# Performance work log

Measured on AMD Instinct MI355X. Metric: run time of the kernel, lower is better.

The kernel has to match this reference:

```python
import jax, jax.numpy as jnp
import numpy as np

TOPK = 2

def setup_inputs() -> dict:
    key = jax.random.key(0)
    k1, k2, k3, k4 = jax.random.split(key, 4)
    T, H, F, E = 2048, 1024, 4096, 8
    x = jax.random.normal(k1, (T, H), dtype=jnp.float32)
    router_weight = jax.random.normal(k2, (H, E), dtype=jnp.float32) * (1.0 / np.sqrt(H))
    w1 = jax.random.normal(k3, (E, H, F), dtype=jnp.float32) * (1.0 / np.sqrt(H))
    w2 = jax.random.normal(k4, (E, F, H), dtype=jnp.float32) * (1.0 / np.sqrt(F))
    return {"x": x, "router_weight": router_weight, "w1": w1, "w2": w2}


def reference(x, router_weight, w1, w2):
    # x: [T, H] tokens; w1: [E, H, F]; w2: [E, F, H]
    T, H = x.shape
    E = w1.shape[0]
    K = TOPK
    M = T * K  # total dispatched token copies

    # --- TopKRouter (Megatron default: top-k over logits, softmax over selected) ---
    logits = x @ router_weight                      # [T, E]
    top_logits, top_idx = jax.lax.top_k(logits, K)  # [T, K]
    probs = jax.nn.softmax(top_logits, axis=-1)     # [T, K]

    # --- AG-scatter: group token copies by expert (flux grouped-GEMM layout) ---
    flat_expert = top_idx.reshape(-1)               # [M], token-major
    token_id = jnp.repeat(jnp.arange(T), K)         # [M]
    order = jnp.argsort(flat_expert)                # stable sort by expert id
    xg = x[token_id[order]]                         # [M, H] grouped inputs
    eg = flat_expert[order]                         # [M] expert of each slot

    # --- grouped GEMM1 + fused GELU, grouped GEMM2 (exact, via expert masking) ---
    # Rows not belonging to expert e are zeroed; gelu(0)=0 and 0@w2=0, so the
    # accumulated buffers are exactly the grouped-GEMM results.
    gelu_buf = jnp.zeros((M, w1.shape[2]), dtype=x.dtype)
    y = jnp.zeros((M, H), dtype=x.dtype)
    for e in range(E):
        mask = (eg == e)[:, None].astype(x.dtype)
        ge = jax.nn.gelu((xg * mask) @ w1[e], approximate=False)  # [M, F]
        gelu_buf = gelu_buf + ge
        y = y + ge @ w2[e]

    # --- gather + reduce: weighted combine of the K expert outputs per token ---
    pg = probs.reshape(-1)[order]                   # [M]
    mlp_output = jax.ops.segment_sum(y * pg[:, None], token_id[order], num_segments=T)
    return (mlp_output, gelu_buf)
```

## Files before the change

### kernel.cpp

```cpp
#include <hip/hip_runtime.h>
#include <hip/hip_bf16.h>
#include <stdint.h>

typedef unsigned short u16;
typedef unsigned int u32;
typedef __attribute__((ext_vector_type(8))) short short8;
typedef __attribute__((ext_vector_type(4))) float f32x4;

#define T_TOK 2048
#define H_DIM 1024
#define F_DIM 4096
#define E_NUM 8
#define M_SLOT 4096
#define MAXTILES 40
#define KSPLIT 2

__device__ __forceinline__ u16 f2bf(float f){
  union { float f; u32 u; } v; v.f = f;
  return (u16)((v.u + 0x7FFFu + ((v.u >> 16) & 1u)) >> 16);
}

__device__ __forceinline__ void gload_lds16(const void* g, void* l){
  __builtin_amdgcn_global_load_lds(
      (const __attribute__((address_space(1))) u32*)g,
      (__attribute__((address_space(3))) u32*)l, 16, 0, 0);
}

__global__ __launch_bounds__(256) void router_kernel(
    const float* __restrict__ x, const float* __restrict__ rw,
    int* __restrict__ tok_e, float* __restrict__ tok_p){
  __shared__ float wlds[E_NUM * H_DIM];
  int tid = threadIdx.x;
  for (int i = tid; i < H_DIM * E_NUM; i += 256){
    int h = i >> 3, e = i & 7;
    wlds[e * H_DIM + h] = rw[i];
  }
  __syncthreads();
  int wave = tid >> 6, lane = tid & 63;
  int t = blockIdx.x * 4 + wave;
  const float* xr = x + (size_t)t * H_DIM;
  float acc[E_NUM];
  #pragma unroll
  for (int e = 0; e < E_NUM; e++) acc[e] = 0.f;
  for (int i = 0; i < H_DIM / 64; i++){
    float xv = xr[lane + 64 * i];
    #pragma unroll
    for (int e = 0; e < E_NUM; e++) acc[e] += xv * wlds[e * H_DIM + lane + 64 * i];
  }
  #pragma unroll
  for (int e = 0; e < E_NUM; e++){
    float r = acc[e];
    #pragma unroll
    for (int off = 32; off; off >>= 1) r += __shfl_xor(r, off, 64);
    acc[e] = r;
  }
  if (lane == 0){
    float l0 = acc[0]; int e0 = 0;
    #pragma unroll
    for (int e = 1; e < E_NUM; e++) if (acc[e] > l0){ l0 = acc[e]; e0 = e; }
    float l1 = -INFINITY; int e1 = 0;
    #pragma unroll
    for (int e = 0; e < E_NUM; e++) if (e != e0 && acc[e] > l1){ l1 = acc[e]; e1 = e; }
    float ex = expf(l1 - l0);
    float inv = 1.f / (1.f + ex);
    tok_e[2*t] = e0; tok_e[2*t+1] = e1;
    tok_p[2*t] = inv; tok_p[2*t+1] = ex * inv;
  }
}

__global__ void hist_kernel(const int* __restrict__ tok_e, u32* __restrict__ partial){
  int lane = threadIdx.x & 63;
  int m = blockIdx.x * 64 + lane;
  int e = tok_e[m];
  #pragma unroll
  for (int ee = 0; ee < E_NUM; ee++){
    unsigned long long mk = __ballot(e == ee);
    if (lane == ee) partial[blockIdx.x * E_NUM + ee] = (u32)__popcll(mk);
  }
}

__global__ void scan_kernel(const u32* __restrict__ partial, u32* __restrict__ baseb,
                            int4* __restrict__ tiles, int* __restrict__ ntiles){
  int lane = threadIdx.x;
  u32 exc[E_NUM], tot[E_NUM];
  #pragma unroll
  for (int e = 0; e < E_NUM; e++){
    u32 v = partial[lane * E_NUM + e];
    u32 own = v;
    #pragma unroll
    for (int off = 1; off < 64; off <<= 1){
      u32 tu = __shfl_up(v, off, 64);
      if (lane >= off) v += tu;
    }
    exc[e] = v - own;
    tot[e] = __shfl(v, 63, 64);
  }
  u32 offs[E_NUM + 1]; offs[0] = 0;
  #pragma unroll
  for (int e = 0; e < E_NUM; e++) offs[e+1] = offs[e] + tot[e];
  #pragma unroll
  for (int e = 0; e < E_NUM; e++) baseb[lane * E_NUM + e] = offs[e] + exc[e];
  if (lane == 0){
    int nt = 0;
    for (int e = 0; e < E_NUM; e++){
      int cnt = (int)tot[e];
      for (int r0 = 0; r0 < cnt; r0 += 128){
        tiles[nt] = make_int4((int)offs[e] + r0, min(128, cnt - r0), e, 0);
        nt++;
      }
    }
    *ntiles = nt;
  }
}

__global__ void scatter_kernel(const int* __restrict__ tok_e, const u32* __restrict__ baseb,
                               int* __restrict__ dest){
  int lane = threadIdx.x & 63;
  int m = blockIdx.x * 64 + lane;
  int e = tok_e[m];
  unsigned long long eq = 0;
  #pragma unroll
  for (int ee = 0; ee < E_NUM; ee++){
    unsigned long long mk = __ballot(e == ee);
    if (e == ee) eq = mk;
  }
  u32 rank = (u32)__popcll(eq & ((1ull << lane) - 1ull));
  dest[m] = (int)(baseb[blockIdx.x * E_NUM + e] + rank);
}

__global__ __launch_bounds__(256) void gather_kernel(const float* __restrict__ x,
                                                     const int* __restrict__ dest,
                                                     u16* __restrict__ xg){
  int m = blockIdx.x;
  int d = dest[m];
  const float4* xr = (const float4*)(x + (size_t)(m >> 1) * H_DIM);
  float4 v = xr[threadIdx.x];
  ushort4 o;
  o.x = f2bf(v.x); o.y = f2bf(v.y); o.z = f2bf(v.z); o.w = f2bf(v.w);
  ((ushort4*)(xg + (size_t)d * H_DIM))[threadIdx.x] = o;
}

template<int R, int C>
__global__ __launch_bounds__(256) void transpose_cvt(const float* __restrict__ in,
                                                     u16* __restrict__ out){
  int e = blockIdx.z;
  const float* ip = in + (size_t)e * R * C;
  u16* op = out + (size_t)e * R * C;
  __shared__ u16 tile[64][66];
  int c0 = blockIdx.x * 64, r0 = blockIdx.y * 64;
  int tr = threadIdx.x >> 4, tc = threadIdx.x & 15;
  #pragma unroll
  for (int i = 0; i < 4; i++){
    int r = tr + i * 16;
    float4 v = *(const float4*)(ip + (size_t)(r0 + r) * C + c0 + tc * 4);
    tile[r][tc*4+0] = f2bf(v.x); tile[r][tc*4+1] = f2bf(v.y);
    tile[r][tc*4+2] = f2bf(v.z); tile[r][tc*4+3] = f2bf(v.w);
  }
  __syncthreads();
  #pragma unroll
  for (int i = 0; i < 4; i++){
    int c = tr + i * 16;
    ushort4 o;
    o.x = tile[tc*4+0][c]; o.y = tile[tc*4+1][c];
    o.z = tile[tc*4+2][c]; o.w = tile[tc*4+3][c];
    *(ushort4*)(op + (size_t)(c0 + c) * R + r0 + tc * 4) = o;
  }
}

template<int N, int KSTRIDE, int NT, bool GELU_EP>
__global__ __launch_bounds__(256, 3) void gemm97(
    const u16* __restrict__ A, const u16* __restrict__ Bt,
    const int4* __restrict__ tiles, const int* __restrict__ ntiles_p,
    float* __restrict__ outF, u16* __restrict__ outB, size_t zstride){
  if ((int)blockIdx.y >= *ntiles_p) return;
  int4 ti = tiles[blockIdx.y];
  int row0 = ti.x, nrows = ti.y, e = ti.z;
  int col0 = blockIdx.x * 128;
  size_t kofs = (size_t)blockIdx.z * ((size_t)NT * 64);
  const u16* Be = Bt + (size_t)e * N * KSTRIDE;
  float* outFz = outF + (size_t)blockIdx.z * zstride;

  __shared__ __align__(16) u16 As[128 * 64];
  __shared__ __align__(16) u16 Bs[128 * 64];
  int lane = threadIdx.x & 63, wid = threadIdx.x >> 6;
  int wr = wid >> 1, wc = wid & 1;

  f32x4 acc[4][4];
  #pragma unroll
  for (int m = 0; m < 4; m++)
    #pragma unroll
    for (int n = 0; n < 4; n++) acc[m][n] = (f32x4)0.f;

  int srow = (wid << 3) + (lane >> 3);
  int skx  = ((lane & 7) * 16) ^ ((lane >> 3) << 4);

  for (int kt = 0; kt < NT; kt++){
    size_t kb = kofs + (size_t)kt * 64;
    #pragma unroll
    for (int i = 0; i < 4; i++){
      int row = i * 32 + srow;
      gload_lds16((const char*)(A  + (size_t)(row0 + row) * KSTRIDE + kb) + skx,
                  As + i * 2048 + wid * 512);
      gload_lds16((const char*)(Be + (size_t)(col0 + row) * KSTRIDE + kb) + skx,
                  Bs + i * 2048 + wid * 512);
    }
    __syncthreads();
    short8 a[4][2], b[4][2];
    #pragma unroll
    for (int m = 0; m < 4; m++){
      int row = wr * 64 + m * 16 + (lane & 15);
      #pragma unroll
      for (int kk = 0; kk < 2; kk++){
        int byte_ = row * 128 + ((kk * 64 + (lane >> 4) * 16) ^ ((row & 7) << 4));
        a[m][kk] = *(const short8*)((const char*)As + byte_);
      }
    }
    #pragma unroll
    for (int n = 0; n < 4; n++){
      int row = wc * 64 + n * 16 + (lane & 15);
      #pragma unroll
      for (int kk = 0; kk < 2; kk++){
        int byte_ = row * 128 + ((kk * 64 + (lane >> 4) * 16) ^ ((row & 7) << 4));
        b[n][kk] = *(const short8*)((const char*)Bs + byte_);
      }
    }
    #pragma unroll
    for (int m = 0; m < 4; m++)
      #pragma unroll
      for (int n = 0; n < 4; n++)
        #pragma unroll
        for (int kk = 0; kk < 2; kk++)
          acc[m][n] = __builtin_amdgcn_mfma_f32_16x16x32_bf16(a[m][kk], b[n][kk], acc[m][n], 0, 0, 0);
    __syncthreads();
  }

  #pragma unroll
  for (int m = 0; m < 4; m++){
    int rloc = wr * 64 + m * 16 + (lane >> 4) * 4;
    #pragma unroll
    for (int j = 0; j < 4; j++){
      int rr = rloc + j;
      if (rr < nrows){
        size_t rowg = (size_t)(row0 + rr);
        #pragma unroll
        for (int n = 0; n < 4; n++){
          int cc = col0 + wc * 64 + n * 16 + (lane & 15);
          float v = acc[m][n][j];
          if (GELU_EP){
            float g = v * 0.5f * (1.f + erff(v * 0.70710678118f));
            outFz[rowg * N + cc] = g;
            outB[rowg * N + cc] = f2bf(g);
          } else {
            outFz[rowg * N + cc] = v;
          }
        }
      }
    }
  }
}

__global__ __launch_bounds__(256) void combine_kernel(const float* __restrict__ yp,
                                                      const int* __restrict__ dest,
                                                      const float* __restrict__ tok_p,
                                                      float* __restrict__ out){
  int t = blockIdx.x;
  int d0 = dest[2*t], d1 = dest[2*t+1];
  float p0 = tok_p[2*t], p1 = tok_p[2*t+1];
  float4 r; r.x = 0.f; r.y = 0.f; r.z = 0.f; r.w = 0.f;
  #pragma unroll
  for (int s = 0; s < KSPLIT; s++){
    float4 a = ((const float4*)(yp + ((size_t)s * M_SLOT + d0) * H_DIM))[threadIdx.x];
    float4 b = ((const float4*)(yp + ((size_t)s * M_SLOT + d1) * H_DIM))[threadIdx.x];
    r.x += p0*a.x + p1*b.x; r.y += p0*a.y + p1*b.y;
    r.z += p0*a.z + p1*b.z; r.w += p0*a.w + p1*b.w;
  }
  ((float4*)(out + (size_t)t * H_DIM))[threadIdx.x] = r;
}

extern "C" void kernel_launch(void* const* d_in, const int* in_sizes, int n_in,
                              void* d_out, int out_size, void* d_ws, size_t ws_size,
                              hipStream_t stream) {
  const float* x  = (const float*)d_in[0];
  const float* rw = (const float*)d_in[1];
  const float* w1 = (const float*)d_in[2];
  const float* w2 = (const float*)d_in[3];
  float* out_mlp  = (float*)d_out;
  float* out_gelu = (float*)d_out + (size_t)T_TOK * H_DIM;

  char* ws = (char*)d_ws;
  u16*   w1t   = (u16*)(ws + 0);
  float* ypart = (float*)(ws + 0);
  u16*   w2t   = (u16*)(ws + 67108864);
  u16*   xg    = (u16*)(ws + 134217728);
  u16*   gb    = (u16*)(ws + 143130624);
  char*  small = ws + 178782208;
  int*   tok_e = (int*)(small);
  float* tok_p = (float*)(small + 16384);
  int*   dest  = (int*)(small + 32768);
  u32*   partial = (u32*)(small + 49152);
  u32*   baseb   = (u32*)(small + 51200);
  int4*  tiles   = (int4*)(small + 53248);
  int*   ntiles  = (int*)(small + 54272);

  router_kernel<<<T_TOK/4, 256, 0, stream>>>(x, rw, tok_e, tok_p);
  hist_kernel<<<M_SLOT/64, 64, 0, stream>>>(tok_e, partial);
  scan_kernel<<<1, 64, 0, stream>>>(partial, baseb, tiles, ntiles);
  scatter_kernel<<<M_SLOT/64, 64, 0, stream>>>(tok_e, baseb, dest);
  gather_kernel<<<M_SLOT, 256, 0, stream>>>(x, dest, xg);
  transpose_cvt<H_DIM, F_DIM><<<dim3(F_DIM/64, H_DIM/64, E_NUM), 256, 0, stream>>>(w1, w1t);
  transpose_cvt<F_DIM, H_DIM><<<dim3(H_DIM/64, F_DIM/64, E_NUM), 256, 0, stream>>>(w2, w2t);
  gemm97<F_DIM, H_DIM, 16, true><<<dim3(F_DIM/128, MAXTILES, 1), 256, 0, stream>>>(
      xg, w1t, tiles, ntiles, out_gelu, gb, 0);
  gemm97<H_DIM, F_DIM, 32, false><<<dim3(H_DIM/128, MAXTILES, KSPLIT), 256, 0, stream>>>(
      gb, w2t, tiles, ntiles, ypart, nullptr, (size_t)M_SLOT * H_DIM);
  combine_kernel<<<T_TOK, 256, 0, stream>>>(ypart, dest, tok_p, out_mlp);
}
```

Measured before the change: 254.0 us.

## Fuse fp32 weight transpose and bf16 conversion into GEMM tile loading

Removes the two standalone transpose/convert kernels. The grouped GEMMs now read fp32 weights directly, convert them to bf16 in registers and write them swizzled into LDS. The main loop becomes register-staged and software-pipelined: the next tile is issued before the MFMAs and committed afterwards. This avoids writing and re-reading 128MB of transposed bf16 weights, but each tile now reads fp32 from global memory (re-read per row tile), and the 32-float register buffer adds pressure that may hurt occupancy.

```diff
diff --git a/kernel.cpp b/kernel.cpp
--- a/kernel.cpp
+++ b/kernel.cpp
@@ -18,12 +18,6 @@
 __device__ __forceinline__ u16 f2bf(float f){
   union { float f; u32 u; } v; v.f = f;
   return (u16)((v.u + 0x7FFFu + ((v.u >> 16) & 1u)) >> 16);
-}
-
-__device__ __forceinline__ void gload_lds16(const void* g, void* l){
-  __builtin_amdgcn_global_load_lds(
-      (const __attribute__((address_space(1))) u32*)g,
-      (__attribute__((address_space(3))) u32*)l, 16, 0, 0);
 }
 
 __global__ __launch_bounds__(256) void router_kernel(
@@ -140,36 +134,9 @@
   ((ushort4*)(xg + (size_t)d * H_DIM))[threadIdx.x] = o;
 }
 
-template<int R, int C>
-__global__ __launch_bounds__(256) void transpose_cvt(const float* __restrict__ in,
-                                                     u16* __restrict__ out){
-  int e = blockIdx.z;
-  const float* ip = in + (size_t)e * R * C;
-  u16* op = out + (size_t)e * R * C;
-  __shared__ u16 tile[64][66];
-  int c0 = blockIdx.x * 64, r0 = blockIdx.y * 64;
-  int tr = threadIdx.x >> 4, tc = threadIdx.x & 15;
-  #pragma unroll
-  for (int i = 0; i < 4; i++){
-    int r = tr + i * 16;
-    float4 v = *(const float4*)(ip + (size_t)(r0 + r) * C + c0 + tc * 4);
-    tile[r][tc*4+0] = f2bf(v.x); tile[r][tc*4+1] = f2bf(v.y);
-    tile[r][tc*4+2] = f2bf(v.z); tile[r][tc*4+3] = f2bf(v.w);
-  }
-  __syncthreads();
-  #pragma unroll
-  for (int i = 0; i < 4; i++){
-    int c = tr + i * 16;
-    ushort4 o;
-    o.x = tile[tc*4+0][c]; o.y = tile[tc*4+1][c];
-    o.z = tile[tc*4+2][c]; o.w = tile[tc*4+3][c];
-    *(ushort4*)(op + (size_t)(c0 + c) * R + r0 + tc * 4) = o;
-  }
-}
-
 template<int N, int KSTRIDE, int NT, bool GELU_EP>
-__global__ __launch_bounds__(256, 3) void gemm97(
-    const u16* __restrict__ A, const u16* __restrict__ Bt,
+__global__ __launch_bounds__(256, 3) void gemmf(
+    const u16* __restrict__ A, const float* __restrict__ W,
     const int4* __restrict__ tiles, const int* __restrict__ ntiles_p,
     float* __restrict__ outF, u16* __restrict__ outB, size_t zstride){
   if ((int)blockIdx.y >= *ntiles_p) return;
@@ -177,7 +144,7 @@
   int row0 = ti.x, nrows = ti.y, e = ti.z;
   int col0 = blockIdx.x * 128;
   size_t kofs = (size_t)blockIdx.z * ((size_t)NT * 64);
-  const u16* Be = Bt + (size_t)e * N * KSTRIDE;
+  const float* We = W + (size_t)e * KSTRIDE * N;
   float* outFz = outF + (size_t)blockIdx.z * zstride;
 
   __shared__ __align__(16) u16 As[128 * 64];
@@ -191,46 +158,67 @@
     #pragma unroll
     for (int n = 0; n < 4; n++) acc[m][n] = (f32x4)0.f;
 
-  int srow = (wid << 3) + (lane >> 3);
-  int skx  = ((lane & 7) * 16) ^ ((lane >> 3) << 4);
+  int skx = ((lane & 7) * 16) ^ ((lane >> 3) << 4);
+  int kh = lane & 1;
+  int nn = wid * 32 + (lane >> 1);
+  int bswz = (nn & 7) << 4;
+
+  short8 areg[4];
+  float breg[32];
+
+  auto issue = [&](int kt){
+    size_t kb = kofs + (size_t)kt * 64;
+    #pragma unroll
+    for (int i = 0; i < 4; i++){
+      int row = i * 32 + (wid << 3) + (lane >> 3);
+      areg[i] = *(const short8*)((const char*)(A + (size_t)(row0 + row) * KSTRIDE + kb) + skx);
+    }
+    const float* gp = We + (kb + (size_t)(kh * 32)) * N + col0 + nn;
+    #pragma unroll
+    for (int j = 0; j < 32; j++) breg[j] = gp[(size_t)j * N];
+  };
+
+  auto commit = [&](){
+    #pragma unroll
+    for (int i = 0; i < 4; i++)
+      *(short8*)((char*)As + i * 4096 + wid * 1024 + lane * 16) = areg[i];
+    #pragma unroll
+    for (int i2 = 0; i2 < 4; i2++){
+      short8 v;
+      #pragma unroll
+      for (int j = 0; j < 8; j++) v[j] = (short)f2bf(breg[i2 * 8 + j]);
+      *(short8*)((char*)Bs + nn * 128 + ((kh * 64 + i2 * 16) ^ bswz)) = v;
+    }
+  };
+
+  issue(0); commit();
+  __syncthreads();
 
   for (int kt = 0; kt < NT; kt++){
-    size_t kb = kofs + (size_t)kt * 64;
-    #pragma unroll
-    for (int i = 0; i < 4; i++){
-      int row = i * 32 + srow;
-      gload_lds16((const char*)(A  + (size_t)(row0 + row) * KSTRIDE + kb) + skx,
-                  As + i * 2048 + wid * 512);
-      gload_lds16((const char*)(Be + (size_t)(col0 + row) * KSTRIDE + kb) + skx,
-                  Bs + i * 2048 + wid * 512);
+    if (kt + 1 < NT) issue(kt + 1);
+    #pragma unroll
+    for (int kk = 0; kk < 2; kk++){
+      short8 a[4], b[4];
+      #pragma unroll
+      for (int m = 0; m < 4; m++){
+        int row = wr * 64 + m * 16 + (lane & 15);
+        int byte_ = row * 128 + ((kk * 64 + (lane >> 4) * 16) ^ ((row & 7) << 4));
+        a[m] = *(const short8*)((const char*)As + byte_);
+      }
+      #pragma unroll
+      for (int n = 0; n < 4; n++){
+        int row = wc * 64 + n * 16 + (lane & 15);
+        int byte_ = row * 128 + ((kk * 64 + (lane >> 4) * 16) ^ ((row & 7) << 4));
+        b[n] = *(const short8*)((const char*)Bs + byte_);
+      }
+      #pragma unroll
+      for (int m = 0; m < 4; m++)
+        #pragma unroll
+        for (int n = 0; n < 4; n++)
+          acc[m][n] = __builtin_amdgcn_mfma_f32_16x16x32_bf16(a[m], b[n], acc[m][n], 0, 0, 0);
     }
     __syncthreads();
-    short8 a[4][2], b[4][2];
-    #pragma unroll
-    for (int m = 0; m < 4; m++){
-      int row = wr * 64 + m * 16 + (lane & 15);
-      #pragma unroll
-      for (int kk = 0; kk < 2; kk++){
-        int byte_ = row * 128 + ((kk * 64 + (lane >> 4) * 16) ^ ((row & 7) << 4));
-        a[m][kk] = *(const short8*)((const char*)As + byte_);
-      }
-    }
-    #pragma unroll
-    for (int n = 0; n < 4; n++){
-      int row = wc * 64 + n * 16 + (lane & 15);
-      #pragma unroll
-      for (int kk = 0; kk < 2; kk++){
-        int byte_ = row * 128 + ((kk * 64 + (lane >> 4) * 16) ^ ((row & 7) << 4));
-        b[n][kk] = *(const short8*)((const char*)Bs + byte_);
-      }
-    }
-    #pragma unroll
-    for (int m = 0; m < 4; m++)
-      #pragma unroll
-      for (int n = 0; n < 4; n++)
-        #pragma unroll
-        for (int kk = 0; kk < 2; kk++)
-          acc[m][n] = __builtin_amdgcn_mfma_f32_16x16x32_bf16(a[m][kk], b[n][kk], acc[m][n], 0, 0, 0);
+    if (kt + 1 < NT) commit();
     __syncthreads();
   }
 
@@ -288,12 +276,10 @@
   float* out_gelu = (float*)d_out + (size_t)T_TOK * H_DIM;
 
   char* ws = (char*)d_ws;
-  u16*   w1t   = (u16*)(ws + 0);
-  float* ypart = (float*)(ws + 0);
-  u16*   w2t   = (u16*)(ws + 67108864);
-  u16*   xg    = (u16*)(ws + 134217728);
-  u16*   gb    = (u16*)(ws + 143130624);
-  char*  small = ws + 178782208;
+  u16*   xg    = (u16*)(ws + 0);
+  u16*   gb    = (u16*)(ws + (9u << 20));
+  float* ypart = (float*)(ws + (48u << 20));
+  char*  small = ws + (84u << 20);
   int*   tok_e = (int*)(small);
   float* tok_p = (float*)(small + 16384);
   int*   dest  = (int*)(small + 32768);
@@ -307,11 +293,9 @@
   scan_kernel<<<1, 64, 0, stream>>>(partial, baseb, tiles, ntiles);
   scatter_kernel<<<M_SLOT/64, 64, 0, stream>>>(tok_e, baseb, dest);
   gather_kernel<<<M_SLOT, 256, 0, stream>>>(x, dest, xg);
-  transpose_cvt<H_DIM, F_DIM><<<dim3(F_DIM/64, H_DIM/64, E_NUM), 256, 0, stream>>>(w1, w1t);
-  transpose_cvt<F_DIM, H_DIM><<<dim3(H_DIM/64, F_DIM/64, E_NUM), 256, 0, stream>>>(w2, w2t);
-  gemm97<F_DIM, H_DIM, 16, true><<<dim3(F_DIM/128, MAXTILES, 1), 256, 0, stream>>>(
-      xg, w1t, tiles, ntiles, out_gelu, gb, 0);
-  gemm97<H_DIM, F_DIM, 32, false><<<dim3(H_DIM/128, MAXTILES, KSPLIT), 256, 0, stream>>>(
-      gb, w2t, tiles, ntiles, ypart, nullptr, (size_t)M_SLOT * H_DIM);
+  gemmf<F_DIM, H_DIM, 16, true><<<dim3(F_DIM/128, MAXTILES, 1), 256, 0, stream>>>(
+      xg, w1, tiles, ntiles, out_gelu, gb, 0);
+  gemmf<H_DIM, F_DIM, 32, false><<<dim3(H_DIM/128, MAXTILES, KSPLIT), 256, 0, stream>>>(
+      gb, w2, tiles, ntiles, ypart, nullptr, (size_t)M_SLOT * H_DIM);
   combine_kernel<<<T_TOK, 256, 0, stream>>>(ypart, dest, tok_p, out_mlp);
 }
```

Result: slower. 308.2 us (+21.3%).

## Fuse weight transposes into gather and GEMM1 launches, raise GEMM2 split-K

Applied to the files above, without the earlier changes.

The w1 transpose is merged into the gather launch, and the w2 transpose runs as extra blocks inside the GEMM1 launch. This lets the bandwidth-bound conversions overlap with other work instead of running as separate serial kernels, and it removes two launches. GEMM2 split-K goes from 2 to 4 with shorter K loops and a launch bound of 4 blocks per CU, which gives more parallelism. The cost is twice as many partial output buffers for the combine kernel to read, and the fused kernels must size shared memory for the larger GEMM path.

```diff
diff --git a/kernel.cpp b/kernel.cpp
--- a/kernel.cpp
+++ b/kernel.cpp
@@ -13,7 +13,7 @@
 #define E_NUM 8
 #define M_SLOT 4096
 #define MAXTILES 40
-#define KSPLIT 2
+#define KSPLIT 4
 
 __device__ __forceinline__ u16 f2bf(float f){
   union { float f; u32 u; } v; v.f = f;
@@ -128,26 +128,14 @@
   dest[m] = (int)(baseb[blockIdx.x * E_NUM + e] + rank);
 }
 
-__global__ __launch_bounds__(256) void gather_kernel(const float* __restrict__ x,
-                                                     const int* __restrict__ dest,
-                                                     u16* __restrict__ xg){
-  int m = blockIdx.x;
-  int d = dest[m];
-  const float4* xr = (const float4*)(x + (size_t)(m >> 1) * H_DIM);
-  float4 v = xr[threadIdx.x];
-  ushort4 o;
-  o.x = f2bf(v.x); o.y = f2bf(v.y); o.z = f2bf(v.z); o.w = f2bf(v.w);
-  ((ushort4*)(xg + (size_t)d * H_DIM))[threadIdx.x] = o;
-}
-
 template<int R, int C>
-__global__ __launch_bounds__(256) void transpose_cvt(const float* __restrict__ in,
-                                                     u16* __restrict__ out){
-  int e = blockIdx.z;
+__device__ __forceinline__ void transpose_body(const float* __restrict__ in,
+                                               u16* __restrict__ out,
+                                               int cx, int ry, int e,
+                                               u16 (*tile)[66]){
   const float* ip = in + (size_t)e * R * C;
   u16* op = out + (size_t)e * R * C;
-  __shared__ u16 tile[64][66];
-  int c0 = blockIdx.x * 64, r0 = blockIdx.y * 64;
+  int c0 = cx * 64, r0 = ry * 64;
   int tr = threadIdx.x >> 4, tc = threadIdx.x & 15;
   #pragma unroll
   for (int i = 0; i < 4; i++){
@@ -168,20 +156,20 @@
 }
 
 template<int N, int KSTRIDE, int NT, bool GELU_EP>
-__global__ __launch_bounds__(256, 3) void gemm97(
+__device__ __forceinline__ void gemm_body(
+    u16* As, u16* Bs,
     const u16* __restrict__ A, const u16* __restrict__ Bt,
     const int4* __restrict__ tiles, const int* __restrict__ ntiles_p,
-    float* __restrict__ outF, u16* __restrict__ outB, size_t zstride){
-  if ((int)blockIdx.y >= *ntiles_p) return;
-  int4 ti = tiles[blockIdx.y];
+    float* __restrict__ outF, u16* __restrict__ outB, size_t zstride,
+    int colBlk, int tileBlk, int z){
+  if (tileBlk >= *ntiles_p) return;
+  int4 ti = tiles[tileBlk];
   int row0 = ti.x, nrows = ti.y, e = ti.z;
-  int col0 = blockIdx.x * 128;
-  size_t kofs = (size_t)blockIdx.z * ((size_t)NT * 64);
+  int col0 = colBlk * 128;
+  size_t kofs = (size_t)z * ((size_t)NT * 64);
   const u16* Be = Bt + (size_t)e * N * KSTRIDE;
-  float* outFz = outF + (size_t)blockIdx.z * zstride;
-
-  __shared__ __align__(16) u16 As[128 * 64];
-  __shared__ __align__(16) u16 Bs[128 * 64];
+  float* outFz = outF + (size_t)z * zstride;
+
   int lane = threadIdx.x & 63, wid = threadIdx.x >> 6;
   int wr = wid >> 1, wc = wid & 1;
 
@@ -259,6 +247,51 @@
   }
 }
 
+__global__ __launch_bounds__(256) void gather_tw1_kernel(
+    const float* __restrict__ x, const int* __restrict__ dest,
+    u16* __restrict__ xg, const float* __restrict__ w1, u16* __restrict__ w1t){
+  __shared__ __align__(16) u16 tile[64][66];
+  int bid = blockIdx.x;
+  if (bid < M_SLOT){
+    int d = dest[bid];
+    const float4* xr = (const float4*)(x + (size_t)(bid >> 1) * H_DIM);
+    float4 v = xr[threadIdx.x];
+    ushort4 o;
+    o.x = f2bf(v.x); o.y = f2bf(v.y); o.z = f2bf(v.z); o.w = f2bf(v.w);
+    ((ushort4*)(xg + (size_t)d * H_DIM))[threadIdx.x] = o;
+  } else {
+    int tb = bid - M_SLOT;
+    transpose_body<H_DIM, F_DIM>(w1, w1t, tb & 63, (tb >> 6) & 15, tb >> 10, tile);
+  }
+}
+
+__global__ __launch_bounds__(256, 4) void gemm1_tw2_kernel(
+    const u16* __restrict__ xg, const u16* __restrict__ w1t,
+    const int4* __restrict__ tiles, const int* __restrict__ ntiles,
+    float* __restrict__ out_gelu, u16* __restrict__ gb,
+    const float* __restrict__ w2, u16* __restrict__ w2t){
+  __shared__ __align__(16) u16 sh[2 * 128 * 64];
+  int bid = blockIdx.x;
+  if (bid < 32 * MAXTILES){
+    gemm_body<F_DIM, H_DIM, 16, true>(sh, sh + 8192, xg, w1t, tiles, ntiles,
+                                      out_gelu, gb, 0, bid & 31, bid >> 5, 0);
+  } else {
+    int tb = bid - 32 * MAXTILES;
+    transpose_body<F_DIM, H_DIM>(w2, w2t, tb & 15, (tb >> 4) & 63, tb >> 10,
+                                 (u16(*)[66])sh);
+  }
+}
+
+__global__ __launch_bounds__(256, 4) void gemm2_kernel(
+    const u16* __restrict__ gb, const u16* __restrict__ w2t,
+    const int4* __restrict__ tiles, const int* __restrict__ ntiles,
+    float* __restrict__ ypart){
+  __shared__ __align__(16) u16 sh[2 * 128 * 64];
+  gemm_body<H_DIM, F_DIM, 16, false>(sh, sh + 8192, gb, w2t, tiles, ntiles,
+                                     ypart, nullptr, (size_t)M_SLOT * H_DIM,
+                                     blockIdx.x, blockIdx.y, blockIdx.z);
+}
+
 __global__ __launch_bounds__(256) void combine_kernel(const float* __restrict__ yp,
                                                       const int* __restrict__ dest,
                                                       const float* __restrict__ tok_p,
@@ -306,12 +339,10 @@
   hist_kernel<<<M_SLOT/64, 64, 0, stream>>>(tok_e, partial);
   scan_kernel<<<1, 64, 0, stream>>>(partial, baseb, tiles, ntiles);
   scatter_kernel<<<M_SLOT/64, 64, 0, stream>>>(tok_e, baseb, dest);
-  gather_kernel<<<M_SLOT, 256, 0, stream>>>(x, dest, xg);
-  transpose_cvt<H_DIM, F_DIM><<<dim3(F_DIM/64, H_DIM/64, E_NUM), 256, 0, stream>>>(w1, w1t);
-  transpose_cvt<F_DIM, H_DIM><<<dim3(H_DIM/64, F_DIM/64, E_NUM), 256, 0, stream>>>(w2, w2t);
-  gemm97<F_DIM, H_DIM, 16, true><<<dim3(F_DIM/128, MAXTILES, 1), 256, 0, stream>>>(
-      xg, w1t, tiles, ntiles, out_gelu, gb, 0);
-  gemm97<H_DIM, F_DIM, 32, false><<<dim3(H_DIM/128, MAXTILES, KSPLIT), 256, 0, stream>>>(
-      gb, w2t, tiles, ntiles, ypart, nullptr, (size_t)M_SLOT * H_DIM);
+  gather_tw1_kernel<<<M_SLOT + 8192, 256, 0, stream>>>(x, dest, xg, w1, w1t);
+  gemm1_tw2_kernel<<<32 * MAXTILES + 8192, 256, 0, stream>>>(
+      xg, w1t, tiles, ntiles, out_gelu, gb, w2, w2t);
+  gemm2_kernel<<<dim3(H_DIM/128, MAXTILES, KSPLIT), 256, 0, stream>>>(
+      gb, w2t, tiles, ntiles, ypart);
   combine_kernel<<<T_TOK, 256, 0, stream>>>(ypart, dest, tok_p, out_mlp);
 }
```

Result: faster. 236.0 us (-7.1%).
